# Performance work log

Measured on AMD Instinct MI355X. Metric: run time of the kernel, lower is better.

Reference implementation:

```python
import jax, jax.numpy as jnp
import numpy as np

KS = 5            # AdaCoF kernel size (ks)
DIL = 1           # dilation
PAD = (KS - 1) * DIL // 2   # ReplicationPad2d amount


def _adacof(frame, weight, alpha, beta):
    """AdaCoF: per-pixel adaptive deformable kernel warp.
    frame:  [B, C, H, W]
    weight/alpha/beta: [B, K2, H, W] with K2 = KS*KS (weight already softmaxed)
    out[b,c,i,j] = sum_k weight[b,k,i,j] * bilerp(frame_pad[b,c],
                     i + (k//KS)*DIL + alpha[b,k,i,j],
                     j + (k%KS)*DIL + beta[b,k,i,j])
    """
    B, C, H, W = frame.shape
    fp = jnp.pad(frame, ((0, 0), (0, 0), (PAD, PAD), (PAD, PAD)), mode='edge')
    Hp, Wp = H + 2 * PAD, W + 2 * PAD
    k = jnp.arange(KS * KS)
    dy = ((k // KS) * DIL).astype(frame.dtype)[:, None, None]   # [K2,1,1]
    dx = ((k % KS) * DIL).astype(frame.dtype)[:, None, None]
    ii = jnp.arange(H, dtype=frame.dtype)[:, None]              # [H,1]
    jj = jnp.arange(W, dtype=frame.dtype)[None, :]              # [1,W]
    y = jnp.clip(alpha + dy + ii, 0.0, Hp - 1.0)                # [B,K2,H,W]
    x = jnp.clip(beta + dx + jj, 0.0, Wp - 1.0)
    y0 = jnp.clip(jnp.floor(y), 0, Hp - 2).astype(jnp.int32)
    x0 = jnp.clip(jnp.floor(x), 0, Wp - 2).astype(jnp.int32)
    fy = (y - y0)[:, None]   # [B,1,K2,H,W]
    fx = (x - x0)[:, None]

    def gather(fpb, y0b, x0b):
        # fpb [C,Hp,Wp]; y0b/x0b [K2,H,W] -> four corners [C,K2,H,W]
        return (fpb[:, y0b, x0b], fpb[:, y0b, x0b + 1],
                fpb[:, y0b + 1, x0b], fpb[:, y0b + 1, x0b + 1])

    v00, v01, v10, v11 = jax.vmap(gather)(fp, y0, x0)  # each [B,C,K2,H,W]
    val = (v00 * (1 - fy) * (1 - fx) + v01 * (1 - fy) * fx
           + v10 * fy * (1 - fx) + v11 * fy * fx)
    return jnp.sum(weight[:, None] * val, axis=2)      # [B,C,H,W]


def setup_inputs() -> dict:
    key = jax.random.key(0)
    k1, k2, k3, k4, k5 = jax.random.split(key, 5)
    T, B, C, H, W = 2, 4, 3, 256, 256
    K2 = KS * KS
    return {
        'frames': jax.random.uniform(k1, (T, B, C, H, W), dtype=jnp.float32),
        'weights': jax.random.normal(k2, (B, T, K2, H, W), dtype=jnp.float32),
        'alphas': jax.random.normal(k3, (B, T, K2, H, W), dtype=jnp.float32),
        'betas': jax.random.normal(k4, (B, T, K2, H, W), dtype=jnp.float32),
        'occ_logits': jax.random.normal(k5, (B, T, H, W), dtype=jnp.float32),
    }


def reference(frames, weights, alphas, betas, occ_logits):
    # Subnet_weight ends with Softmax over the ks^2 channel dim.
    w = jax.nn.softmax(weights, axis=2)
    # moduleOcclusion ends with Softmax over the n_inputs (T) dim.
    occ = jax.nn.softmax(occ_logits, axis=1)
    T = frames.shape[0]
    out = jnp.zeros_like(frames[0])
    for t in range(T):  # small fixed T=2
        out = out + occ[:, t, None] * _adacof(frames[t], w[:, t], alphas[:, t], betas[:, t])
    return out
```

## Files before the change

kernel.cpp:

```cpp
#include <hip/hip_runtime.h>
#include <hip/hip_bf16.h>


#define KS 5
#define K2 25
#define PADR 2

constexpr int T_ = 2;
constexpr int B_ = 4;
constexpr int C_ = 3;
constexpr int H_ = 256;
constexpr int W_ = 256;
constexpr int HW_ = H_ * W_;
constexpr int BCHW_ = B_ * C_ * HW_;
constexpr float HP_MAX = (float)(H_ + 2 * PADR - 1);
constexpr float WP_MAX = (float)(W_ + 2 * PADR - 1);
constexpr float HP_M2 = (float)(H_ + 2 * PADR - 2);
constexpr float WP_M2 = (float)(W_ + 2 * PADR - 2);

constexpr int TILE_W = 32;
constexpr int TILE_H = 8;
constexpr int HALO   = 8;
constexpr int RPAD   = HALO + PADR;
constexpr int WROWS  = TILE_H + 21;
constexpr int WCOLS  = TILE_W + 21;
constexpr int PLANE  = WROWS * WCOLS;
constexpr int NTILE  = HW_ / (TILE_W * TILE_H);

__global__ __launch_bounds__(256) void adacof_tile(
    const float* __restrict__ frames,
    const float* __restrict__ weights,
    const float* __restrict__ alphas,
    const float* __restrict__ betas,
    const float* __restrict__ occl,
    float* __restrict__ part)
{
    __shared__ float win[3 * PLANE];

    const int bid  = blockIdx.x;
    const int b    = bid >> 9;
    const int rem  = bid & 511;
    const int t    = rem & 1;
    const int tile = rem >> 1;
    const int i0   = (tile >> 3) << 3;
    const int j0   = (tile & 7) << 5;

    const int tid = threadIdx.x;
    const int wy0 = i0 - RPAD;
    const int wx0 = j0 - RPAD;

    const float* __restrict__ fb = frames + (size_t)(t * B_ + b) * C_ * HW_;

    #pragma unroll
    for (int c = 0; c < 3; ++c) {
        for (int e = tid; e < PLANE; e += 256) {
            const int wy = e / WCOLS;
            const int wx = e - wy * WCOLS;
            const int gy = min(max(wy0 + wy, 0), H_ - 1);
            const int gx = min(max(wx0 + wx, 0), W_ - 1);
            win[c * PLANE + e] = fb[c * HW_ + (gy << 8) + gx];
        }
    }

    const int x = tid & 31, r = tid >> 5;
    const int i = i0 + r, j = j0 + x;
    const int ij = (i << 8) | j;

    const int btbase = ((b * T_ + t) * K2) * HW_ + ij;
    const float* __restrict__ wp = weights + btbase;
    const float* __restrict__ ap = alphas + btbase;
    const float* __restrict__ bp = betas + btbase;

    const float o_own = occl[(b * T_ + t) * HW_ + ij];
    const float o_oth = occl[(b * T_ + (1 - t)) * HW_ + ij];

    __syncthreads();

    float wsum = 0.0f, acc0 = 0.0f, acc1 = 0.0f, acc2 = 0.0f;
    const float fi = (float)i;
    const float fj = (float)j;

    #pragma unroll
    for (int k = 0; k < K2; ++k) {
        const float wv = wp[k * HW_];
        const float av = ap[k * HW_];
        const float bv = bp[k * HW_];
        const float ew = __expf(wv);
        wsum += ew;

        const int kd = k / KS;
        const float dy = (float)kd;
        const float dx = (float)(k - kd * KS);

        float y  = fminf(fmaxf(av + dy + fi, 0.0f), HP_MAX);
        float xx = fminf(fmaxf(bv + dx + fj, 0.0f), WP_MAX);
        float y0f = fminf(floorf(y), HP_M2);
        float x0f = fminf(floorf(xx), WP_M2);
        const int y0 = (int)y0f;
        const int x0 = (int)x0f;
        float fx = xx - x0f;
        float fy = y - y0f;
        fx = (x0 <= 1) ? 0.0f : ((x0 >= W_ + 1) ? 1.0f : fx);
        fy = (y0 <= 1) ? 0.0f : ((y0 >= H_ + 1) ? 1.0f : fy);
        const int lx = min(max(x0 - PADR, 0), W_ - 2);
        const int ly = min(max(y0 - PADR, 0), H_ - 2);

        const int wyr = min(max(ly - wy0, 0), WROWS - 2);
        const int wxr = min(max(lx - wx0, 0), WCOLS - 2);
        const int l = wyr * WCOLS + wxr;

        const float w00 = (1.0f - fy) * (1.0f - fx) * ew;
        const float w01 = (1.0f - fy) * fx * ew;
        const float w10 = fy * (1.0f - fx) * ew;
        const float w11 = fy * fx * ew;

        acc0 += w00 * win[l]             + w01 * win[l + 1]
              + w10 * win[l + WCOLS]     + w11 * win[l + WCOLS + 1];
        acc1 += w00 * win[PLANE + l]         + w01 * win[PLANE + l + 1]
              + w10 * win[PLANE + l + WCOLS] + w11 * win[PLANE + l + WCOLS + 1];
        acc2 += w00 * win[2 * PLANE + l]         + w01 * win[2 * PLANE + l + 1]
              + w10 * win[2 * PLANE + l + WCOLS] + w11 * win[2 * PLANE + l + WCOLS + 1];
    }

    const float occw = 1.0f / (1.0f + __expf(o_oth - o_own));
    const float wscale = occw / wsum;

    float* __restrict__ pt = part + ((size_t)(t * B_ + b) * C_) * HW_ + ij;
    pt[0]       = acc0 * wscale;
    pt[HW_]     = acc1 * wscale;
    pt[2 * HW_] = acc2 * wscale;
}

__global__ void combine2(const float4* __restrict__ part, float4* __restrict__ out) {
    const int n = blockIdx.x * blockDim.x + threadIdx.x;
    const float4 p0 = part[n];
    const float4 p1 = part[n + BCHW_ / 4];
    float4 r;
    r.x = p0.x + p1.x; r.y = p0.y + p1.y; r.z = p0.z + p1.z; r.w = p0.w + p1.w;
    out[n] = r;
}

extern "C" void kernel_launch(void* const* d_in, const int* in_sizes, int n_in,
                              void* d_out, int out_size, void* d_ws, size_t ws_size,
                              hipStream_t stream) {
    const float* frames  = (const float*)d_in[0];
    const float* weights = (const float*)d_in[1];
    const float* alphas  = (const float*)d_in[2];
    const float* betas   = (const float*)d_in[3];
    const float* occl    = (const float*)d_in[4];
    float* out = (float*)d_out;
    float* part = (float*)d_ws;

    const int blocks = B_ * T_ * NTILE;
    adacof_tile<<<blocks, 256, 0, stream>>>(frames, weights, alphas, betas,
                                            occl, part);
    combine2<<<(BCHW_ / 4) / 256, 256, 0, stream>>>((const float4*)part,
                                                    (float4*)out);
}
```

Baseline: 41.16 us.

## Interleave channels 0/1 in LDS as float2 and prefetch softmax weights before barrier

Stores the shared-memory window with channels 0 and 1 interleaved as float2, so each bilinear corner needs one 64-bit LDS read for two channels plus one scalar read for the third. It also issues all 25 weight loads and their exps before the barrier, overlapping that global latency with the tile fill. Accumulation is rewritten as explicit fma chains. This raises register pressure (25 extra live floats), which could lower occupancy, and float2 LDS access may change bank-conflict behaviour.

```diff
diff --git a/kernel.cpp b/kernel.cpp
--- a/kernel.cpp
+++ b/kernel.cpp
@@ -35,7 +35,8 @@
     const float* __restrict__ occl,
     float* __restrict__ part)
 {
-    __shared__ float win[3 * PLANE];
+    __shared__ float2 win01[PLANE];
+    __shared__ float  win2[PLANE];
 
     const int bid  = blockIdx.x;
     const int b    = bid >> 9;
@@ -51,15 +52,14 @@
 
     const float* __restrict__ fb = frames + (size_t)(t * B_ + b) * C_ * HW_;
 
-    #pragma unroll
-    for (int c = 0; c < 3; ++c) {
-        for (int e = tid; e < PLANE; e += 256) {
-            const int wy = e / WCOLS;
-            const int wx = e - wy * WCOLS;
-            const int gy = min(max(wy0 + wy, 0), H_ - 1);
-            const int gx = min(max(wx0 + wx, 0), W_ - 1);
-            win[c * PLANE + e] = fb[c * HW_ + (gy << 8) + gx];
-        }
+    for (int e = tid; e < PLANE; e += 256) {
+        const int wy = e / WCOLS;
+        const int wx = e - wy * WCOLS;
+        const int gy = min(max(wy0 + wy, 0), H_ - 1);
+        const int gx = min(max(wx0 + wx, 0), W_ - 1);
+        const int g = (gy << 8) + gx;
+        win01[e] = make_float2(fb[g], fb[HW_ + g]);
+        win2[e]  = fb[2 * HW_ + g];
     }
 
     const int x = tid & 31, r = tid >> 5;
@@ -74,19 +74,27 @@
     const float o_own = occl[(b * T_ + t) * HW_ + ij];
     const float o_oth = occl[(b * T_ + (1 - t)) * HW_ + ij];
 
+    float pw[K2];
+    #pragma unroll
+    for (int k = 0; k < K2; ++k) pw[k] = wp[k * HW_];
+    float wsum = 0.0f;
+    #pragma unroll
+    for (int k = 0; k < K2; ++k) {
+        pw[k] = __expf(pw[k]);
+        wsum += pw[k];
+    }
+
     __syncthreads();
 
-    float wsum = 0.0f, acc0 = 0.0f, acc1 = 0.0f, acc2 = 0.0f;
+    float2 acc01 = make_float2(0.0f, 0.0f);
+    float acc2 = 0.0f;
     const float fi = (float)i;
     const float fj = (float)j;
 
     #pragma unroll
     for (int k = 0; k < K2; ++k) {
-        const float wv = wp[k * HW_];
         const float av = ap[k * HW_];
         const float bv = bp[k * HW_];
-        const float ew = __expf(wv);
-        wsum += ew;
 
         const int kd = k / KS;
         const float dy = (float)kd;
@@ -109,25 +117,31 @@
         const int wxr = min(max(lx - wx0, 0), WCOLS - 2);
         const int l = wyr * WCOLS + wxr;
 
+        const float ew = pw[k];
         const float w00 = (1.0f - fy) * (1.0f - fx) * ew;
         const float w01 = (1.0f - fy) * fx * ew;
         const float w10 = fy * (1.0f - fx) * ew;
         const float w11 = fy * fx * ew;
 
-        acc0 += w00 * win[l]             + w01 * win[l + 1]
-              + w10 * win[l + WCOLS]     + w11 * win[l + WCOLS + 1];
-        acc1 += w00 * win[PLANE + l]         + w01 * win[PLANE + l + 1]
-              + w10 * win[PLANE + l + WCOLS] + w11 * win[PLANE + l + WCOLS + 1];
-        acc2 += w00 * win[2 * PLANE + l]         + w01 * win[2 * PLANE + l + 1]
-              + w10 * win[2 * PLANE + l + WCOLS] + w11 * win[2 * PLANE + l + WCOLS + 1];
+        const float2 p00 = win01[l];
+        const float2 p01 = win01[l + 1];
+        const float2 p10 = win01[l + WCOLS];
+        const float2 p11 = win01[l + WCOLS + 1];
+        acc01.x = fmaf(w00, p00.x, fmaf(w01, p01.x,
+                  fmaf(w10, p10.x, fmaf(w11, p11.x, acc01.x))));
+        acc01.y = fmaf(w00, p00.y, fmaf(w01, p01.y,
+                  fmaf(w10, p10.y, fmaf(w11, p11.y, acc01.y))));
+
+        acc2 = fmaf(w00, win2[l], fmaf(w01, win2[l + 1],
+               fmaf(w10, win2[l + WCOLS], fmaf(w11, win2[l + WCOLS + 1], acc2))));
     }
 
     const float occw = 1.0f / (1.0f + __expf(o_oth - o_own));
     const float wscale = occw / wsum;
 
     float* __restrict__ pt = part + ((size_t)(t * B_ + b) * C_) * HW_ + ij;
-    pt[0]       = acc0 * wscale;
-    pt[HW_]     = acc1 * wscale;
+    pt[0]       = acc01.x * wscale;
+    pt[HW_]     = acc01.y * wscale;
     pt[2 * HW_] = acc2 * wscale;
 }
 
```

Result: slower. 43.69 us (+6.2%).

## Fuse both time steps into one 512-thread block and drop combine kernel

Applied to the files above, without the earlier changes.

Each block now covers both input frames for one tile: threads 0-255 handle t=0 and 256-511 handle t=1, each half with its own shared-memory window. The t=1 results go through shared memory and are added to the t=0 results before a single write to the output. This removes the partial-sum workspace round trip and the second kernel launch. In exchange it doubles block size and shared memory per block, which may lower occupancy, and adds two block-wide barriers.

```diff
diff --git a/kernel.cpp b/kernel.cpp
--- a/kernel.cpp
+++ b/kernel.cpp
@@ -12,7 +12,6 @@
 constexpr int H_ = 256;
 constexpr int W_ = 256;
 constexpr int HW_ = H_ * W_;
-constexpr int BCHW_ = B_ * C_ * HW_;
 constexpr float HP_MAX = (float)(H_ + 2 * PADR - 1);
 constexpr float WP_MAX = (float)(W_ + 2 * PADR - 1);
 constexpr float HP_M2 = (float)(H_ + 2 * PADR - 2);
@@ -27,42 +26,44 @@
 constexpr int PLANE  = WROWS * WCOLS;
 constexpr int NTILE  = HW_ / (TILE_W * TILE_H);
 
-__global__ __launch_bounds__(256) void adacof_tile(
+__global__ __launch_bounds__(512) void adacof_pair(
     const float* __restrict__ frames,
     const float* __restrict__ weights,
     const float* __restrict__ alphas,
     const float* __restrict__ betas,
     const float* __restrict__ occl,
-    float* __restrict__ part)
+    float* __restrict__ out)
 {
-    __shared__ float win[3 * PLANE];
+    __shared__ float win[2 * 3 * PLANE];
 
     const int bid  = blockIdx.x;
-    const int b    = bid >> 9;
-    const int rem  = bid & 511;
-    const int t    = rem & 1;
-    const int tile = rem >> 1;
+    const int b    = bid >> 8;
+    const int tile = bid & 255;
     const int i0   = (tile >> 3) << 3;
     const int j0   = (tile & 7) << 5;
 
     const int tid = threadIdx.x;
+    const int t   = tid >> 8;
+    const int lt  = tid & 255;
+
     const int wy0 = i0 - RPAD;
     const int wx0 = j0 - RPAD;
 
+    float* __restrict__ winT = win + t * (3 * PLANE);
     const float* __restrict__ fb = frames + (size_t)(t * B_ + b) * C_ * HW_;
 
     #pragma unroll
     for (int c = 0; c < 3; ++c) {
-        for (int e = tid; e < PLANE; e += 256) {
+        for (int e = lt; e < PLANE; e += 256) {
             const int wy = e / WCOLS;
             const int wx = e - wy * WCOLS;
             const int gy = min(max(wy0 + wy, 0), H_ - 1);
             const int gx = min(max(wx0 + wx, 0), W_ - 1);
-            win[c * PLANE + e] = fb[c * HW_ + (gy << 8) + gx];
+            winT[c * PLANE + e] = fb[c * HW_ + (gy << 8) + gx];
         }
     }
 
-    const int x = tid & 31, r = tid >> 5;
+    const int x = lt & 31, r = lt >> 5;
     const int i = i0 + r, j = j0 + x;
     const int ij = (i << 8) | j;
 
@@ -114,30 +115,34 @@
         const float w10 = fy * (1.0f - fx) * ew;
         const float w11 = fy * fx * ew;
 
-        acc0 += w00 * win[l]             + w01 * win[l + 1]
-              + w10 * win[l + WCOLS]     + w11 * win[l + WCOLS + 1];
-        acc1 += w00 * win[PLANE + l]         + w01 * win[PLANE + l + 1]
-              + w10 * win[PLANE + l + WCOLS] + w11 * win[PLANE + l + WCOLS + 1];
-        acc2 += w00 * win[2 * PLANE + l]         + w01 * win[2 * PLANE + l + 1]
-              + w10 * win[2 * PLANE + l + WCOLS] + w11 * win[2 * PLANE + l + WCOLS + 1];
+        acc0 += w00 * winT[l]             + w01 * winT[l + 1]
+              + w10 * winT[l + WCOLS]     + w11 * winT[l + WCOLS + 1];
+        acc1 += w00 * winT[PLANE + l]         + w01 * winT[PLANE + l + 1]
+              + w10 * winT[PLANE + l + WCOLS] + w11 * winT[PLANE + l + WCOLS + 1];
+        acc2 += w00 * winT[2 * PLANE + l]         + w01 * winT[2 * PLANE + l + 1]
+              + w10 * winT[2 * PLANE + l + WCOLS] + w11 * winT[2 * PLANE + l + WCOLS + 1];
     }
 
     const float occw = 1.0f / (1.0f + __expf(o_oth - o_own));
     const float wscale = occw / wsum;
+    const float r0 = acc0 * wscale;
+    const float r1 = acc1 * wscale;
+    const float r2 = acc2 * wscale;
 
-    float* __restrict__ pt = part + ((size_t)(t * B_ + b) * C_) * HW_ + ij;
-    pt[0]       = acc0 * wscale;
-    pt[HW_]     = acc1 * wscale;
-    pt[2 * HW_] = acc2 * wscale;
-}
-
-__global__ void combine2(const float4* __restrict__ part, float4* __restrict__ out) {
-    const int n = blockIdx.x * blockDim.x + threadIdx.x;
-    const float4 p0 = part[n];
-    const float4 p1 = part[n + BCHW_ / 4];
-    float4 r;
-    r.x = p0.x + p1.x; r.y = p0.y + p1.y; r.z = p0.z + p1.z; r.w = p0.w + p1.w;
-    out[n] = r;
+    __syncthreads();
+    float* __restrict__ exch = win;
+    if (t == 1) {
+        exch[lt * 3 + 0] = r0;
+        exch[lt * 3 + 1] = r1;
+        exch[lt * 3 + 2] = r2;
+    }
+    __syncthreads();
+    if (t == 0) {
+        float* __restrict__ op = out + (size_t)(b * C_) * HW_ + ij;
+        op[0]       = r0 + exch[lt * 3 + 0];
+        op[HW_]     = r1 + exch[lt * 3 + 1];
+        op[2 * HW_] = r2 + exch[lt * 3 + 2];
+    }
 }
 
 extern "C" void kernel_launch(void* const* d_in, const int* in_sizes, int n_in,
@@ -149,11 +154,8 @@
     const float* betas   = (const float*)d_in[3];
     const float* occl    = (const float*)d_in[4];
     float* out = (float*)d_out;
-    float* part = (float*)d_ws;
 
-    const int blocks = B_ * T_ * NTILE;
-    adacof_tile<<<blocks, 256, 0, stream>>>(frames, weights, alphas, betas,
-                                            occl, part);
-    combine2<<<(BCHW_ / 4) / 256, 256, 0, stream>>>((const float4*)part,
-                                                    (float4*)out);
+    const int blocks = B_ * NTILE;
+    adacof_pair<<<blocks, 512, 0, stream>>>(frames, weights, alphas, betas,
+                                            occl, out);
 }
```

New measurement: 45.68 us. +11.0%, slower.
